# Kernel tuning notes

Hardware: AMD Instinct MI355X
Metric: run time of the kernel (lower is better)

Reference implementation:

```python
import jax, jax.numpy as jnp
import numpy as np


def _conv1x1(x, w, b):
    # x: (B,C,H,W), w: (O,C), b: (O,)
    return jnp.einsum('oc,bchw->bohw', w, x) + b[None, :, None, None]


def _avg_pool2(x):
    B, C, H, W = x.shape
    return x.reshape(B, C, H // 2, 2, W // 2, 2).mean(axis=(3, 5))


def setup_inputs() -> dict:
    key = jax.random.key(0)
    B, C, H, W = 8, 64, 64, 64
    ks = jax.random.split(key, 14)
    s = 1.0 / np.sqrt(C)

    def wb(k1, k2):
        return (jax.random.uniform(k1, (C, C), jnp.float32, -s, s),
                jax.random.uniform(k2, (C,), jnp.float32, -s, s))

    w_q, b_q = wb(ks[0], ks[1])
    w_K, b_K = wb(ks[2], ks[3])
    w_V, b_V = wb(ks[4], ks[5])
    w_Q, b_Q = wb(ks[6], ks[7])
    w_k, b_k = wb(ks[8], ks[9])
    w_v, b_v = wb(ks[10], ks[11])
    x = jax.random.normal(ks[12], (B, C, H, W), jnp.float32)
    gamma = jnp.ones((1,), jnp.float32)
    return dict(x=x, w_q=w_q, b_q=b_q, w_K=w_K, b_K=b_K, w_V=w_V, b_V=b_V,
                w_Q=w_Q, b_Q=b_Q, w_k=w_k, b_k=b_k, w_v=w_v, b_v=b_v,
                gamma=gamma)


def reference(x, w_q, b_q, w_K, b_K, w_V, b_V, w_Q, b_Q, w_k, b_k, w_v, b_v, gamma):
    B, C, H, W = x.shape
    N = H * W
    N4 = N // 4

    # Stage 1: pooled queries vs full key/value
    q = _conv1x1(x, w_q, b_q)                      # (B,C,H,W); torch views as (B,C,W,H) but H==W
    qp = _avg_pool2(q).reshape(B, C, N4).transpose(0, 2, 1)   # (B,N/4,C)
    Kf = _conv1x1(x, w_K, b_K).reshape(B, C, N)                # (B,C,N)
    Vf = _conv1x1(x, w_V, b_V).reshape(B, C, N)                # (B,C,N)
    attn = jax.nn.softmax(jnp.einsum('bnc,bcm->bnm', qp, Kf), axis=-1)  # (B,N/4,N)
    out = jnp.einsum('bcm,bnm->bcn', Vf, attn)                 # (B,C,N/4)
    out = out.reshape(B, C, H // 2, W // 2)

    # Stage 2: full queries vs pooled-derived key/value
    Qf = _conv1x1(x, w_Q, b_Q).reshape(B, C, N).transpose(0, 2, 1)  # (B,N,C)
    kp = _conv1x1(out, w_k, b_k).reshape(B, C, N4)                  # (B,C,N/4)
    vp = _conv1x1(out, w_v, b_v).reshape(B, C, N4)                  # (B,C,N/4)
    attn2 = jax.nn.softmax(jnp.einsum('bnc,bcm->bnm', Qf, kp), axis=-1)  # (B,N,N/4)
    out2 = jnp.einsum('bcm,bnm->bcn', vp, attn2).reshape(B, C, H, W)

    return gamma * out2 + x
```

## Files before the change

### kernel.cpp

```cpp
#include <hip/hip_runtime.h>
#include <math.h>


typedef __bf16 bf16;
typedef __attribute__((ext_vector_type(4))) __bf16 bf16x4;
typedef __attribute__((ext_vector_type(8))) __bf16 bf16x8;
typedef __attribute__((ext_vector_type(4))) float f32x4;

__device__ __forceinline__ void gl_lds16(const bf16* g, bf16* l) {
    __builtin_amdgcn_global_load_lds(
        (const __attribute__((address_space(1))) unsigned int*)g,
        (__attribute__((address_space(3))) unsigned int*)l,
        16, 0, 0);
}

struct WFrag { bf16x8 f[4][2]; };

template<int WT>
__device__ __forceinline__ WFrag load_wfrag(const float* __restrict__ W, int lane) {
    const int c16 = lane & 15, q4 = lane >> 4;
    WFrag wf;
    #pragma unroll
    for (int to = 0; to < 4; ++to)
        #pragma unroll
        for (int h = 0; h < 2; ++h) {
            bf16 tmp[8];
            if (WT == 0) {
                const float* wp = W + (16 * to + c16) * 64 + q4 * 8 + 32 * h;
                float4 f0 = *(const float4*)wp;
                float4 f1 = *(const float4*)(wp + 4);
                tmp[0] = (bf16)f0.x; tmp[1] = (bf16)f0.y;
                tmp[2] = (bf16)f0.z; tmp[3] = (bf16)f0.w;
                tmp[4] = (bf16)f1.x; tmp[5] = (bf16)f1.y;
                tmp[6] = (bf16)f1.z; tmp[7] = (bf16)f1.w;
            } else {
                #pragma unroll
                for (int j = 0; j < 8; ++j)
                    tmp[j] = (bf16)W[(q4 * 8 + 32 * h + j) * 64 + 16 * to + c16];
            }
            wf.f[to][h] = *(bf16x8*)tmp;
        }
    return wf;
}

template<int OUT>
__device__ __forceinline__ void proj_run(
    const bf16* __restrict__ src, int TN, const WFrag& wf, const float* __restrict__ Bs,
    bf16* __restrict__ Y, int N, int b, int gn0, bf16* __restrict__ Yl, int lane)
{
    const int c16 = lane & 15, q4 = lane >> 4;
    for (int tn = 0; tn < TN; ++tn) {
        bf16x8 xb0 = *(const bf16x8*)&src[(16 * tn + c16) * 72 + q4 * 8];
        bf16x8 xb1 = *(const bf16x8*)&src[(16 * tn + c16) * 72 + q4 * 8 + 32];
        #pragma unroll
        for (int to = 0; to < 4; ++to) {
            f32x4 acc = (f32x4){0.f, 0.f, 0.f, 0.f};
            acc = __builtin_amdgcn_mfma_f32_16x16x32_bf16(wf.f[to][0], xb0, acc, 0, 0, 0);
            acc = __builtin_amdgcn_mfma_f32_16x16x32_bf16(wf.f[to][1], xb1, acc, 0, 0, 0);
            float bias[4] = {0.f, 0.f, 0.f, 0.f};
            if (Bs) {
                float4 b4 = *(const float4*)(Bs + 16 * to + q4 * 4);
                bias[0] = b4.x; bias[1] = b4.y; bias[2] = b4.z; bias[3] = b4.w;
            }
            if (OUT == 0) {
                bf16x4 yv;
                #pragma unroll
                for (int r = 0; r < 4; ++r) yv[r] = (bf16)(acc[r] + bias[r]);
                *(bf16x4*)(Y + ((size_t)b * N + gn0 + 16 * tn + c16) * 64 + 16 * to + 4 * q4) = yv;
            } else if (OUT == 1) {
                #pragma unroll
                for (int r = 0; r < 4; ++r)
                    Y[((size_t)b * 64 + 16 * to + 4 * q4 + r) * N + gn0 + 16 * tn + c16] =
                        (bf16)(acc[r] + bias[r]);
            } else {
                bf16x4 yv;
                #pragma unroll
                for (int r = 0; r < 4; ++r) yv[r] = (bf16)(acc[r] + bias[r]);
                *(bf16x4*)&Yl[(16 * tn + c16) * 72 + 16 * to + 4 * q4] = yv;
            }
        }
    }
}

__global__ __launch_bounds__(256) void prep_kernel(
    const float* __restrict__ x,
    const float* __restrict__ w_q, const float* __restrict__ b_q,
    const float* __restrict__ w_K,
    bf16* __restrict__ xt, bf16* __restrict__ xn, bf16* __restrict__ qkt)
{
    __shared__ float tile[128 * 65];
    __shared__ __align__(16) bf16 xpb[32 * 72];
    __shared__ __align__(16) bf16 qtile[32 * 72];
    const int t  = threadIdx.x;
    const int h2 = blockIdx.x;
    const int b  = blockIdx.y;
    const int n0 = h2 * 128;

    #pragma unroll
    for (int i = 0; i < 32; ++i) {
        int lin = i * 256 + t;
        int n = lin & 127, c = lin >> 7;
        tile[n * 65 + c] = x[((size_t)b * 64 + c) * 4096 + n0 + n];
    }
    __syncthreads();
    {
        int wp = t & 31, c0 = (t >> 5) * 8;
        bf16 tmp[8];
        #pragma unroll
        for (int j = 0; j < 8; ++j) {
            float a = tile[(2 * wp) * 65 + c0 + j] + tile[(2 * wp + 1) * 65 + c0 + j]
                    + tile[(64 + 2 * wp) * 65 + c0 + j] + tile[(64 + 2 * wp + 1) * 65 + c0 + j];
            tmp[j] = (bf16)(0.25f * a);
        }
        *(bf16x8*)&xpb[wp * 72 + c0] = *(bf16x8*)tmp;
    }
    __syncthreads();

    #pragma unroll
    for (int i = 0; i < 4; ++i) {
        int slot = i * 256 + t;
        int n = slot >> 3, c0 = (slot & 7) * 8;
        bf16 tmp[8];
        #pragma unroll
        for (int j = 0; j < 8; ++j) tmp[j] = (bf16)tile[n * 65 + c0 + j];
        *(bf16x8*)&xt[((size_t)b * 4096 + n0 + n) * 64 + c0] = *(bf16x8*)tmp;
    }
    #pragma unroll
    for (int i = 0; i < 4; ++i) {
        int slot = i * 256 + t;
        int c = slot >> 4, n8 = slot & 15;
        bf16 tmp[8];
        #pragma unroll
        for (int j = 0; j < 8; ++j) tmp[j] = (bf16)tile[(n8 * 8 + j) * 65 + c];
        *(bf16x8*)&xn[((size_t)b * 64 + c) * 4096 + n0 + n8 * 8] = *(bf16x8*)tmp;
    }
    if ((t >> 6) == 3) {
        const int lane = t & 63;
        WFrag wfq  = load_wfrag<0>(w_q, lane);
        WFrag wfKT = load_wfrag<1>(w_K, lane);
        proj_run<2>(xpb, 2, wfq, b_q, nullptr, 0, 0, 0, qtile, lane);
        asm volatile("s_waitcnt lgkmcnt(0)" ::: "memory");
        proj_run<0>(qtile, 2, wfKT, nullptr, qkt, 1024, b, h2 * 32, nullptr, lane);
    }
}

template<int NSPLIT, int MODE, int U, int KS, bool BIAS>
__global__ __launch_bounds__(256 * KS, KS == 1 ? 3 : 2) void flash_kernel(
    const bf16* __restrict__ Qt, const bf16* __restrict__ Kt,
    const bf16* __restrict__ Vn, int NQ, int L,
    bf16* __restrict__ Opart, float* __restrict__ Lbuf,
    float* __restrict__ out_f, const float* __restrict__ resid,
    const float* __restrict__ gamma_p, const float* __restrict__ Gb)
{
    const int tid  = threadIdx.x;
    const int lane = tid & 63;
    const int w    = tid >> 6;
    const int wl   = w & 3;
    const int g    = w >> 2;
    const int c16  = lane & 15;
    const int q4   = lane >> 4;
    const int b    = blockIdx.y;
    const int n0   = blockIdx.x * (64 * U) + wl * (16 * U);
    const int s    = (NSPLIT > 1) ? blockIdx.z : 0;
    const int SL   = L / (NSPLIT * KS);
    const int k0   = (s * KS + g) * SL;
    const int ntiles = SL / 64;

    __shared__ __align__(16) bf16 Ks[KS][2][64 * 64];
    __shared__ __align__(16) bf16 Vs[KS][2][64 * 64];
    __shared__ __align__(16) bf16 Pw[4 * KS][16 * U * 72];

    const int rl8 = lane >> 3;
    const int cg  = ((lane & 7) - rl8) & 7;

    const bf16* Kb = Kt + (size_t)b * L * 64;
    const bf16* Vb = Vn + (size_t)b * 64 * L;

    bf16x8 bq[U][2];
    #pragma unroll
    for (int u = 0; u < U; ++u) {
        const bf16* qrow = Qt + ((size_t)b * NQ + n0 + 16 * u + c16) * 64 + q4 * 8;
        bq[u][0] = *(const bf16x8*)(qrow);
        bq[u][1] = *(const bf16x8*)(qrow + 32);
    }

    f32x4 O[U][4];
    #pragma unroll
    for (int u = 0; u < U; ++u)
        #pragma unroll
        for (int gi = 0; gi < 4; ++gi) O[u][gi] = (f32x4){0.f, 0.f, 0.f, 0.f};
    float l_acc[U];
    #pragma unroll
    for (int u = 0; u < U; ++u) l_acc[u] = 0.f;

    #pragma unroll
    for (int j = 0; j < 2; ++j) {
        const int row = 16 * wl + 8 * j + rl8;
        gl_lds16(Kb + (size_t)(k0 + row) * 64 + cg * 8, &Ks[g][0][(16 * wl + 8 * j) * 64]);
        gl_lds16(Vb + (size_t)row * L + k0 + cg * 8,    &Vs[g][0][(16 * wl + 8 * j) * 64]);
    }
    __syncthreads();

    for (int it = 0; it < ntiles; ++it) {
        const int buf = it & 1;
        if (it + 1 < ntiles) {
            const int kn = k0 + (it + 1) * 64;
            #pragma unroll
            for (int j = 0; j < 2; ++j) {
                const int row = 16 * wl + 8 * j + rl8;
                gl_lds16(Kb + (size_t)(kn + row) * 64 + cg * 8, &Ks[g][buf ^ 1][(16 * wl + 8 * j) * 64]);
                gl_lds16(Vb + (size_t)row * L + kn + cg * 8,    &Vs[g][buf ^ 1][(16 * wl + 8 * j) * 64]);
            }
        }

        f32x4 sv[U][4];
        #pragma unroll
        for (int t = 0; t < 4; ++t) {
            const bf16* krow = &Ks[g][buf][(16 * t + c16) * 64];
            bf16x8 ak0 = *(const bf16x8*)&krow[((q4 + c16) & 7) * 8];
            bf16x8 ak1 = *(const bf16x8*)&krow[((q4 + 4 + c16) & 7) * 8];
            #pragma unroll
            for (int u = 0; u < U; ++u) {
                f32x4 z = (f32x4){0.f, 0.f, 0.f, 0.f};
                z = __builtin_amdgcn_mfma_f32_16x16x32_bf16(ak0, bq[u][0], z, 0, 0, 0);
                sv[u][t] = __builtin_amdgcn_mfma_f32_16x16x32_bf16(ak1, bq[u][1], z, 0, 0, 0);
            }
        }

        float4 gb[4];
        if (BIAS) {
            #pragma unroll
            for (int t = 0; t < 4; ++t)
                gb[t] = *(const float4*)&Gb[(size_t)b * 1024 + k0 + it * 64 + 16 * t + 4 * q4];
        }

        #pragma unroll
        for (int u = 0; u < U; ++u) {
            #pragma unroll
            for (int t = 0; t < 4; ++t) {
                #pragma unroll
                for (int r = 0; r < 4; ++r) {
                    float sval = sv[u][t][r];
                    if (BIAS) sval += ((const float*)&gb[t])[r];
                    float p = __expf(sval);
                    sv[u][t][r] = p;
                    l_acc[u] += p;
                }
                bf16x4 pv;
                pv[0] = (bf16)sv[u][t][0]; pv[1] = (bf16)sv[u][t][1];
                pv[2] = (bf16)sv[u][t][2]; pv[3] = (bf16)sv[u][t][3];
                *(bf16x4*)&Pw[w][(16 * u + c16) * 72 + 16 * t + 4 * q4] = pv;
            }
        }

        #pragma unroll
        for (int h = 0; h < 2; ++h) {
            bf16x8 pf[U];
            #pragma unroll
            for (int u = 0; u < U; ++u)
                pf[u] = *(const bf16x8*)&Pw[w][(16 * u + c16) * 72 + 32 * h + 8 * q4];
            #pragma unroll
            for (int gi = 0; gi < 4; ++gi) {
                bf16x8 av = *(const bf16x8*)&Vs[g][buf][(16 * gi + c16) * 64 + ((4 * h + q4 + c16) & 7) * 8];
                #pragma unroll
                for (int u = 0; u < U; ++u)
                    O[u][gi] = __builtin_amdgcn_mfma_f32_16x16x32_bf16(av, pf[u], O[u][gi], 0, 0, 0);
            }
        }
        __syncthreads();
    }

    float l_tot[U];
    #pragma unroll
    for (int u = 0; u < U; ++u) {
        float l = l_acc[u];
        l += __shfl_xor(l, 16);
        l += __shfl_xor(l, 32);
        l_tot[u] = l;
    }

    if (KS == 2) {
        float* sc = (float*)&Pw[0][0];
        const int base = (wl * 64 + lane) * 34;
        if (g == 1) {
            #pragma unroll
            for (int u = 0; u < U; ++u) {
                #pragma unroll
                for (int gi = 0; gi < 4; ++gi)
                    #pragma unroll
                    for (int r = 0; r < 4; ++r)
                        sc[base + u * 16 + gi * 4 + r] = O[u][gi][r];
                sc[base + 32 + u] = l_tot[u];
            }
        }
        __syncthreads();
        if (g == 1) return;
        #pragma unroll
        for (int u = 0; u < U; ++u) {
            #pragma unroll
            for (int gi = 0; gi < 4; ++gi)
                #pragma unroll
                for (int r = 0; r < 4; ++r)
                    O[u][gi][r] += sc[base + u * 16 + gi * 4 + r];
            l_tot[u] += sc[base + 32 + u];
        }
    }

    if (MODE == 2) {
        const float gm = gamma_p[0];
        #pragma unroll
        for (int u = 0; u < U; ++u) {
            float inv = gm / l_tot[u];
            const int n = n0 + 16 * u + c16;
            #pragma unroll
            for (int gi = 0; gi < 4; ++gi) {
                #pragma unroll
                for (int r = 0; r < 4; ++r) {
                    size_t oidx = ((size_t)b * 64 + 16 * gi + 4 * q4 + r) * NQ + n;
                    out_f[oidx] = O[u][gi][r] * inv + resid[oidx];
                }
            }
        }
    } else {
        #pragma unroll
        for (int u = 0; u < U; ++u) {
            float inv = 1.0f / l_tot[u];
            bf16* dst = Opart + ((size_t)(b * NSPLIT + s) * NQ + n0 + 16 * u + c16) * 64 + q4 * 4;
            #pragma unroll
            for (int gi = 0; gi < 4; ++gi) {
                bf16x4 yv;
                #pragma unroll
                for (int r = 0; r < 4; ++r) yv[r] = (bf16)(O[u][gi][r] * inv);
                *(bf16x4*)(dst + 16 * gi) = yv;
            }
        }
        if (lane < 16) {
            #pragma unroll
            for (int u = 0; u < U; ++u)
                Lbuf[(b * NSPLIT + s) * NQ + n0 + 16 * u + lane] = l_tot[u];
        }
    }
}

__global__ __launch_bounds__(256) void comb1kv_kernel(
    const bf16* __restrict__ Opart, const float* __restrict__ Lbuf,
    const float* __restrict__ w_V, const float* __restrict__ b_V,
    const float* __restrict__ w_k, const float* __restrict__ b_k,
    const float* __restrict__ w_v, const float* __restrict__ b_v,
    const float* __restrict__ w_Q, const float* __restrict__ b_Q,
    bf16* __restrict__ qk2t, bf16* __restrict__ vp, float* __restrict__ Gb)
{
    __shared__ __align__(16) bf16 tile[32 * 72];
    __shared__ __align__(16) bf16 otile[32 * 72];
    __shared__ __align__(16) bf16 kpl[32 * 72];
    __shared__ float wbuf[32 * 8];
    const int t  = threadIdx.x;
    const int m0 = blockIdx.x * 32;
    const int b  = blockIdx.y;
    const int w  = t >> 6;
    const int lane = t & 63;

    WFrag wf;
    if      (w == 0) wf = load_wfrag<0>(w_V, lane);
    else if (w == 1) wf = load_wfrag<0>(w_k, lane);
    else if (w == 2) wf = load_wfrag<0>(w_v, lane);
    else             wf = load_wfrag<1>(w_Q, lane);

    if (t < 32) {
        int m = m0 + t;
        float ls[8], lt = 0.f;
        #pragma unroll
        for (int s = 0; s < 8; ++s) {
            ls[s] = Lbuf[(b * 8 + s) * 1024 + m];
            lt += ls[s];
        }
        float inv = 1.f / lt;
        #pragma unroll
        for (int s = 0; s < 8; ++s) wbuf[t * 8 + s] = ls[s] * inv;
    }
    __syncthreads();

    #pragma unroll
    for (int i = 0; i < 2; ++i) {
        int ml = i * 16 + (t >> 4);
        int c4 = (t & 15) * 4;
        const bf16* base = Opart + ((size_t)(b * 8) * 1024 + m0 + ml) * 64 + c4;
        float a0 = 0.f, a1 = 0.f, a2 = 0.f, a3 = 0.f;
        #pragma unroll
        for (int s = 0; s < 8; ++s) {
            bf16x4 v = *(const bf16x4*)(base + (size_t)s * 1024 * 64);
            float wg = wbuf[ml * 8 + s];
            a0 += (float)v[0] * wg; a1 += (float)v[1] * wg;
            a2 += (float)v[2] * wg; a3 += (float)v[3] * wg;
        }
        bf16x4 o; o[0] = (bf16)a0; o[1] = (bf16)a1; o[2] = (bf16)a2; o[3] = (bf16)a3;
        *(bf16x4*)&tile[ml * 72 + c4] = o;
    }
    __syncthreads();

    if (w == 0) proj_run<2>(tile, 2, wf, b_V, nullptr, 0, 0, 0, otile, lane);
    __syncthreads();
    if (w == 1) proj_run<2>(otile, 2, wf, b_k, nullptr, 0, 0, 0, kpl, lane);
    if (w == 2) proj_run<1>(otile, 2, wf, b_v, vp, 1024, b, m0, nullptr, lane);
    __syncthreads();
    if (w == 3) proj_run<0>(kpl, 2, wf, nullptr, qk2t, 1024, b, m0, nullptr, lane);
    if (w == 0 && lane < 32) {
        float acc = 0.f;
        #pragma unroll
        for (int c = 0; c < 64; ++c) acc += b_Q[c] * (float)kpl[lane * 72 + c];
        Gb[(size_t)b * 1024 + m0 + lane] = acc;
    }
}

extern "C" void kernel_launch(void* const* d_in, const int* in_sizes, int n_in,
                              void* d_out, int out_size, void* d_ws, size_t ws_size,
                              hipStream_t stream) {
    const float* x    = (const float*)d_in[0];
    const float* w_q  = (const float*)d_in[1];
    const float* b_q  = (const float*)d_in[2];
    const float* w_K  = (const float*)d_in[3];
    const float* b_K  = (const float*)d_in[4];   (void)b_K;
    const float* w_V  = (const float*)d_in[5];
    const float* b_V  = (const float*)d_in[6];
    const float* w_Q  = (const float*)d_in[7];
    const float* b_Q  = (const float*)d_in[8];
    const float* w_k  = (const float*)d_in[9];
    const float* b_k  = (const float*)d_in[10];
    const float* w_v  = (const float*)d_in[11];
    const float* b_v  = (const float*)d_in[12];
    const float* gamma = (const float*)d_in[13];
    float* out = (float*)d_out;

    char* ws = (char*)d_ws;
    bf16*  xt    = (bf16*)ws;   ws += (size_t)8 * 4096 * 64 * 2;
    bf16*  xn    = (bf16*)ws;   ws += (size_t)8 * 4096 * 64 * 2;
    bf16*  qkt   = (bf16*)ws;   ws += (size_t)8 * 1024 * 64 * 2;
    bf16*  qk2t  = (bf16*)ws;   ws += (size_t)8 * 1024 * 64 * 2;
    bf16*  vp    = (bf16*)ws;   ws += (size_t)8 * 64 * 1024 * 2;
    bf16*  Opart = (bf16*)ws;   ws += (size_t)8 * 8 * 1024 * 64 * 2;
    float* Lb    = (float*)ws;  ws += (size_t)8 * 8 * 1024 * 4;
    float* Gb    = (float*)ws;  ws += (size_t)8 * 1024 * 4;

    prep_kernel<<<dim3(32, 8), 256, 0, stream>>>(x, w_q, b_q, w_K, xt, xn, qkt);

    flash_kernel<8, 1, 2, 1, false><<<dim3(8, 8, 8), 256, 0, stream>>>(
        qkt, xt, xn, 1024, 4096, Opart, Lb, nullptr, nullptr, nullptr, nullptr);

    comb1kv_kernel<<<dim3(32, 8), 256, 0, stream>>>(
        Opart, Lb, w_V, b_V, w_k, b_k, w_v, b_v, w_Q, b_Q, qk2t, vp, Gb);

    flash_kernel<1, 2, 2, 2, true><<<dim3(32, 8, 1), 512, 0, stream>>>(
        xt, qk2t, vp, 4096, 1024, nullptr, nullptr, out, x, gamma, Gb);
}
```

Baseline: 135.0 us.

## Repack softmax probabilities in registers via permlane swaps instead of LDS round-trip

Replaces the per-wave LDS staging buffer for the P matrix with in-register conversion (v_cvt_pk_bf16_f32) and cross-lane permutes (v_permlane32/16_swap) that produce the MFMA B-operand layout directly. This removes LDS writes and reads of P on every tile and frees that shared memory, which may raise occupancy. The scratch area used for the KS==2 reduction is now carved from the K/V buffer region. It relies on the exact lane mapping of the permlane swaps and on gfx950-specific instructions.

```diff
diff --git a/kernel.cpp b/kernel.cpp
--- a/kernel.cpp
+++ b/kernel.cpp
@@ -12,6 +12,18 @@
         (const __attribute__((address_space(1))) unsigned int*)g,
         (__attribute__((address_space(3))) unsigned int*)l,
         16, 0, 0);
+}
+
+__device__ __forceinline__ unsigned cvtpk(float a, float b) {
+    unsigned r;
+    asm("v_cvt_pk_bf16_f32 %0, %1, %2" : "=v"(r) : "v"(a), "v"(b));
+    return r;
+}
+__device__ __forceinline__ void swap32(unsigned &a, unsigned &b) {
+    asm("v_permlane32_swap_b32 %0, %1" : "+v"(a), "+v"(b));
+}
+__device__ __forceinline__ void swap16(unsigned &a, unsigned &b) {
+    asm("v_permlane16_swap_b32 %0, %1" : "+v"(a), "+v"(b));
 }
 
 struct WFrag { bf16x8 f[4][2]; };
@@ -166,9 +178,9 @@
     const int k0   = (s * KS + g) * SL;
     const int ntiles = SL / 64;
 
-    __shared__ __align__(16) bf16 Ks[KS][2][64 * 64];
-    __shared__ __align__(16) bf16 Vs[KS][2][64 * 64];
-    __shared__ __align__(16) bf16 Pw[4 * KS][16 * U * 72];
+    __shared__ __align__(16) char smem[(size_t)KS * 2 * 4096 * 2 * 2];
+    bf16* Ksm = (bf16*)smem;
+    bf16* Vsm = (bf16*)(smem + (size_t)KS * 2 * 4096 * 2);
 
     const int rl8 = lane >> 3;
     const int cg  = ((lane & 7) - rl8) & 7;
@@ -196,8 +208,8 @@
     #pragma unroll
     for (int j = 0; j < 2; ++j) {
         const int row = 16 * wl + 8 * j + rl8;
-        gl_lds16(Kb + (size_t)(k0 + row) * 64 + cg * 8, &Ks[g][0][(16 * wl + 8 * j) * 64]);
-        gl_lds16(Vb + (size_t)row * L + k0 + cg * 8,    &Vs[g][0][(16 * wl + 8 * j) * 64]);
+        gl_lds16(Kb + (size_t)(k0 + row) * 64 + cg * 8, &Ksm[(g * 2 + 0) * 4096 + (16 * wl + 8 * j) * 64]);
+        gl_lds16(Vb + (size_t)row * L + k0 + cg * 8,    &Vsm[(g * 2 + 0) * 4096 + (16 * wl + 8 * j) * 64]);
     }
     __syncthreads();
 
@@ -208,15 +220,17 @@
             #pragma unroll
             for (int j = 0; j < 2; ++j) {
                 const int row = 16 * wl + 8 * j + rl8;
-                gl_lds16(Kb + (size_t)(kn + row) * 64 + cg * 8, &Ks[g][buf ^ 1][(16 * wl + 8 * j) * 64]);
-                gl_lds16(Vb + (size_t)row * L + kn + cg * 8,    &Vs[g][buf ^ 1][(16 * wl + 8 * j) * 64]);
+                gl_lds16(Kb + (size_t)(kn + row) * 64 + cg * 8,
+                         &Ksm[(g * 2 + (buf ^ 1)) * 4096 + (16 * wl + 8 * j) * 64]);
+                gl_lds16(Vb + (size_t)row * L + kn + cg * 8,
+                         &Vsm[(g * 2 + (buf ^ 1)) * 4096 + (16 * wl + 8 * j) * 64]);
             }
         }
 
         f32x4 sv[U][4];
         #pragma unroll
         for (int t = 0; t < 4; ++t) {
-            const bf16* krow = &Ks[g][buf][(16 * t + c16) * 64];
+            const bf16* krow = &Ksm[(g * 2 + buf) * 4096 + (16 * t + c16) * 64];
             bf16x8 ak0 = *(const bf16x8*)&krow[((q4 + c16) & 7) * 8];
             bf16x8 ak1 = *(const bf16x8*)&krow[((q4 + 4 + c16) & 7) * 8];
             #pragma unroll
@@ -234,10 +248,11 @@
                 gb[t] = *(const float4*)&Gb[(size_t)b * 1024 + k0 + it * 64 + 16 * t + 4 * q4];
         }
 
+        bf16x8 pfs[U][2];
         #pragma unroll
         for (int u = 0; u < U; ++u) {
             #pragma unroll
-            for (int t = 0; t < 4; ++t) {
+            for (int t = 0; t < 4; ++t)
                 #pragma unroll
                 for (int r = 0; r < 4; ++r) {
                     float sval = sv[u][t][r];
@@ -246,25 +261,34 @@
                     sv[u][t][r] = p;
                     l_acc[u] += p;
                 }
-                bf16x4 pv;
-                pv[0] = (bf16)sv[u][t][0]; pv[1] = (bf16)sv[u][t][1];
-                pv[2] = (bf16)sv[u][t][2]; pv[3] = (bf16)sv[u][t][3];
-                *(bf16x4*)&Pw[w][(16 * u + c16) * 72 + 16 * t + 4 * q4] = pv;
-            }
+            unsigned A0 = cvtpk(sv[u][0][0], sv[u][0][1]);
+            unsigned A1 = cvtpk(sv[u][0][2], sv[u][0][3]);
+            unsigned A2 = cvtpk(sv[u][2][0], sv[u][2][1]);
+            unsigned A3 = cvtpk(sv[u][2][2], sv[u][2][3]);
+            unsigned B0 = cvtpk(sv[u][1][0], sv[u][1][1]);
+            unsigned B1 = cvtpk(sv[u][1][2], sv[u][1][3]);
+            unsigned B2 = cvtpk(sv[u][3][0], sv[u][3][1]);
+            unsigned B3 = cvtpk(sv[u][3][2], sv[u][3][3]);
+            swap32(A0, B0); swap16(A0, B0);
+            swap32(A1, B1); swap16(A1, B1);
+            swap32(A2, B2); swap16(A2, B2);
+            swap32(A3, B3); swap16(A3, B3);
+            union { unsigned wd[4]; bf16x8 v; } p0, p1;
+            p0.wd[0] = A0; p0.wd[1] = A1; p0.wd[2] = B0; p0.wd[3] = B1;
+            p1.wd[0] = A2; p1.wd[1] = A3; p1.wd[2] = B2; p1.wd[3] = B3;
+            pfs[u][0] = p0.v;
+            pfs[u][1] = p1.v;
         }
 
         #pragma unroll
         for (int h = 0; h < 2; ++h) {
-            bf16x8 pf[U];
-            #pragma unroll
-            for (int u = 0; u < U; ++u)
-                pf[u] = *(const bf16x8*)&Pw[w][(16 * u + c16) * 72 + 32 * h + 8 * q4];
             #pragma unroll
             for (int gi = 0; gi < 4; ++gi) {
-                bf16x8 av = *(const bf16x8*)&Vs[g][buf][(16 * gi + c16) * 64 + ((4 * h + q4 + c16) & 7) * 8];
+                bf16x8 av = *(const bf16x8*)&Vsm[(g * 2 + buf) * 4096 +
+                                                 (16 * gi + c16) * 64 + ((4 * h + q4 + c16) & 7) * 8];
                 #pragma unroll
                 for (int u = 0; u < U; ++u)
-                    O[u][gi] = __builtin_amdgcn_mfma_f32_16x16x32_bf16(av, pf[u], O[u][gi], 0, 0, 0);
+                    O[u][gi] = __builtin_amdgcn_mfma_f32_16x16x32_bf16(av, pfs[u][h], O[u][gi], 0, 0, 0);
             }
         }
         __syncthreads();
@@ -280,7 +304,7 @@
     }
 
     if (KS == 2) {
-        float* sc = (float*)&Pw[0][0];
+        float* sc = (float*)smem;
         const int base = (wl * 64 + lane) * 34;
         if (g == 1) {
             #pragma unroll
```

Result: no change. 132.7 us (-1.7%).
